# Kernel tuning notes

Hardware: AMD Instinct MI355X
Metric: run time of the kernel (lower is better)

## Reference

```python
import jax, jax.numpy as jnp
import numpy as np

N_HEADS = 16


def setup_inputs() -> dict:
    key = jax.random.key(0)
    k1, k2, k3 = jax.random.split(key, 3)
    B, S, D = 2, 2048, 1024
    x = jax.random.normal(k1, (B, S, D), dtype=jnp.float32)
    w_qkv = jax.random.normal(k2, (D, 3 * D), dtype=jnp.float32) * 0.02
    b_qkv = jnp.zeros((3 * D,), dtype=jnp.float32)
    w_proj = jax.random.normal(k3, (D, D), dtype=jnp.float32) * 0.02
    b_proj = jnp.zeros((D,), dtype=jnp.float32)
    return {"x": x, "w_qkv": w_qkv, "b_qkv": b_qkv, "w_proj": w_proj, "b_proj": b_proj}


def reference(x, w_qkv, b_qkv, w_proj, b_proj):
    # Faithful to CausalAttention.flash_atttention: the blockwise online-softmax
    # loop computes exactly softmax(Q K^T / sqrt(hd) + causal_mask) V (no dropout).
    B, S, D = x.shape
    H = N_HEADS
    hd = D // H
    scale = 1.0 / jnp.sqrt(jnp.asarray(hd, dtype=x.dtype))

    qkv = x @ w_qkv + b_qkv                       # [B, S, 3D]
    q, k, v = jnp.split(qkv, 3, axis=-1)
    q = q.reshape(B, S, H, hd).transpose(0, 2, 1, 3)  # [B, H, S, hd]
    k = k.reshape(B, S, H, hd).transpose(0, 2, 1, 3)
    v = v.reshape(B, S, H, hd).transpose(0, 2, 1, 3)

    scores = jnp.einsum('bhqd,bhkd->bhqk', q, k) * scale  # [B, H, S, S]
    causal = jnp.tril(jnp.ones((S, S), dtype=bool))
    scores = jnp.where(causal, scores, -jnp.inf)
    attn = jax.nn.softmax(scores, axis=-1)
    out = jnp.einsum('bhqk,bhkd->bhqd', attn, v)  # [B, H, S, hd]
    out = out.transpose(0, 2, 1, 3).reshape(B, S, D)
    return out @ w_proj + b_proj
```

## Files before the change

### kernel.cpp

```cpp
#include <hip/hip_runtime.h>
#include <hip/hip_bf16.h>

typedef unsigned short u16;
typedef __attribute__((ext_vector_type(8))) short short8;
typedef __attribute__((ext_vector_type(4))) float floatx4;
typedef __attribute__((ext_vector_type(16))) float floatx16;

__device__ __forceinline__ u16 f2bf(float f) {
  union { float f; unsigned u; } v; v.f = f;
  unsigned r = v.u + 0x7fffu + ((v.u >> 16) & 1u);
  return (u16)(r >> 16);
}

__device__ __forceinline__ floatx4 mfma16(short8 a, short8 b, floatx4 c) {
  return __builtin_amdgcn_mfma_f32_16x16x32_bf16(a, b, c, 0, 0, 0);
}
__device__ __forceinline__ floatx16 mfma32(short8 a, short8 b, floatx16 c) {
  return __builtin_amdgcn_mfma_f32_32x32x16_bf16(a, b, c, 0, 0, 0);
}

#define AS1 __attribute__((address_space(1)))
#define AS3 __attribute__((address_space(3)))
__device__ __forceinline__ void gload_lds16(const u16* g, u16* l) {
  __builtin_amdgcn_global_load_lds((const AS1 void*)g, (AS3 void*)l, 16, 0, 0);
}

__device__ __forceinline__ unsigned pack2(float a, float b) {
  union { __hip_bfloat162 h; unsigned u; } x;
  x.h = __hip_bfloat162(__float2bfloat16(a), __float2bfloat16(b));
  return x.u;
}

__device__ __forceinline__ float fexp2(float x) {
#if __has_builtin(__builtin_amdgcn_exp2f)
  return __builtin_amdgcn_exp2f(x);
#else
  return exp2f(x);
#endif
}

#define WAIT_VM(N) asm volatile("s_waitcnt vmcnt(" #N ")" ::: "memory")
#define BARRIER()                      \
  do {                                 \
    __builtin_amdgcn_s_barrier();      \
    asm volatile("" ::: "memory");     \
  } while (0)

#define QSCALE 0.18033688f

__global__ void __launch_bounds__(256) f32_to_bf16_vec(
    const float* __restrict__ in, u16* __restrict__ out) {
  const int i = blockIdx.x * 256 + threadIdx.x;
  const float4* p = (const float4*)in + (size_t)i * 2;
  float4 a = p[0], b = p[1];
  short8 o;
  o[0] = (short)f2bf(a.x); o[1] = (short)f2bf(a.y);
  o[2] = (short)f2bf(a.z); o[3] = (short)f2bf(a.w);
  o[4] = (short)f2bf(b.x); o[5] = (short)f2bf(b.y);
  o[6] = (short)f2bf(b.z); o[7] = (short)f2bf(b.w);
  *(short8*)(out + (size_t)i * 8) = o;
}

__global__ void __launch_bounds__(256) transpose_f32_to_bf16(
    const float* __restrict__ in, u16* __restrict__ out, int R, int C) {
  __shared__ float tile[64][65];
  const int c0 = blockIdx.x * 64, r0 = blockIdx.y * 64;
  const int t = threadIdx.x;
  const int rr = t >> 2, cc = (t & 3) * 16;
  const float* src = in + (size_t)(r0 + rr) * C + (c0 + cc);
  float4 v0 = *(const float4*)(src);
  float4 v1 = *(const float4*)(src + 4);
  float4 v2 = *(const float4*)(src + 8);
  float4 v3 = *(const float4*)(src + 12);
  tile[rr][cc + 0] = v0.x;  tile[rr][cc + 1] = v0.y;
  tile[rr][cc + 2] = v0.z;  tile[rr][cc + 3] = v0.w;
  tile[rr][cc + 4] = v1.x;  tile[rr][cc + 5] = v1.y;
  tile[rr][cc + 6] = v1.z;  tile[rr][cc + 7] = v1.w;
  tile[rr][cc + 8] = v2.x;  tile[rr][cc + 9] = v2.y;
  tile[rr][cc + 10] = v2.z; tile[rr][cc + 11] = v2.w;
  tile[rr][cc + 12] = v3.x; tile[rr][cc + 13] = v3.y;
  tile[rr][cc + 14] = v3.z; tile[rr][cc + 15] = v3.w;
  __syncthreads();
  short8 w0, w1;
#pragma unroll
  for (int i = 0; i < 8; ++i) {
    w0[i] = (short)f2bf(tile[cc + i][rr]);
    w1[i] = (short)f2bf(tile[cc + 8 + i][rr]);
  }
  u16* dst = out + (size_t)(c0 + rr) * R + (r0 + cc);
  *(short8*)dst = w0;
  *(short8*)(dst + 8) = w1;
}

__global__ void __launch_bounds__(256) gemm_qkv(
    const u16* __restrict__ A, const u16* __restrict__ Bt,
    const float* __restrict__ bias, u16* __restrict__ O0,
    u16* __restrict__ O1, u16* __restrict__ O2, int N, int K) {
  __shared__ u16 As[2][4096];
  __shared__ u16 Bs[2][4096];
  const int t = threadIdx.x, w = t >> 6, l = t & 63;
  const int lo = l & 15, g = l >> 4;
  const int wr = w >> 1, wc = w & 1;
  const int m0 = blockIdx.y * 128, n0 = blockIdx.x * 128;
  const int srow = l >> 2;
  const int schunk = (l & 3) ^ ((l >> 4) & 3);
  const u16* ApS = A + (size_t)(m0 + w * 32 + srow) * K + schunk * 8;
  const u16* BpS = Bt + (size_t)(n0 + w * 32 + srow) * K + schunk * 8;

  floatx4 acc[4][4] = {};
  const int NT = K >> 5;

#define STAGE_G(buf, kt_)                                                    \
  do {                                                                       \
    const size_t k0_ = (size_t)(kt_) * 32;                                   \
    _Pragma("unroll") for (int i = 0; i < 2; ++i)                            \
        gload_lds16(ApS + (size_t)i * 16 * K + k0_,                          \
                    &As[buf][(w * 2 + i) * 512]);                            \
    _Pragma("unroll") for (int i = 0; i < 2; ++i)                            \
        gload_lds16(BpS + (size_t)i * 16 * K + k0_,                          \
                    &Bs[buf][(w * 2 + i) * 512]);                            \
  } while (0)

#define COMPUTE_G(cur)                                                       \
  do {                                                                       \
    short8 af[4], bff[4];                                                    \
    _Pragma("unroll") for (int m = 0; m < 4; ++m) {                          \
      const int row = wr * 64 + m * 16 + lo;                                 \
      const int sl = g ^ ((lo >> 2) & 3);                                    \
      af[m] = *(const short8*)(&As[cur][row * 32 + sl * 8]);                 \
    }                                                                        \
    _Pragma("unroll") for (int n = 0; n < 4; ++n) {                          \
      const int row = wc * 64 + n * 16 + lo;                                 \
      const int sl = g ^ ((lo >> 2) & 3);                                    \
      bff[n] = *(const short8*)(&Bs[cur][row * 32 + sl * 8]);                \
    }                                                                        \
    __builtin_amdgcn_s_setprio(1);                                           \
    _Pragma("unroll") for (int m = 0; m < 4; ++m)                            \
        _Pragma("unroll") for (int n = 0; n < 4; ++n) acc[m][n] =            \
            mfma16(af[m], bff[n], acc[m][n]);                                \
    __builtin_amdgcn_s_setprio(0);                                           \
  } while (0)

  STAGE_G(0, 0);
  int cur = 0;
  for (int kt = 0; kt < NT - 1; ++kt) {
    STAGE_G(cur ^ 1, kt + 1);
    WAIT_VM(4);
    BARRIER();
    COMPUTE_G(cur);
    BARRIER();
    cur ^= 1;
  }
  WAIT_VM(0);
  BARRIER();
  COMPUTE_G(cur);
#undef STAGE_G
#undef COMPUTE_G

#pragma unroll
  for (int m = 0; m < 4; ++m) {
    const int row_base = m0 + wr * 64 + m * 16 + g * 4;
#pragma unroll
    for (int n = 0; n < 4; ++n) {
      const int col = n0 + wc * 64 + n * 16 + lo;
      const float bv = bias[col];
#pragma unroll
      for (int j = 0; j < 4; ++j) {
        const int r = row_base + j;
        const float v = acc[m][n][j] + bv;
        const int b = r >> 11, s = r & 2047;
        int c = col;
        if (c < 1024) {
          const int hh = c >> 6, d = c & 63;
          O0[(((size_t)(b * 16 + hh)) * 2048 + s) * 64 + d] = f2bf(v * QSCALE);
        } else if (c < 2048) {
          c -= 1024;
          const int hh = c >> 6, d = c & 63;
          O1[(((size_t)(b * 16 + hh)) * 2048 + s) * 64 + d] = f2bf(v);
        } else {
          c -= 2048;
          const int hh = c >> 6, d = c & 63;
          O2[(((size_t)(b * 16 + hh)) * 64 + d) * 2048 + s] = f2bf(v);
        }
      }
    }
  }
}

__global__ void __launch_bounds__(256, 2) gemm_proj(
    const u16* __restrict__ A, const u16* __restrict__ Bt,
    const float* __restrict__ bias, float* __restrict__ Of, int N, int K) {
  __shared__ u16 As[2][8192];
  __shared__ u16 Bs[2][8192];
  const int t = threadIdx.x, w = t >> 6, l = t & 63;
  const int lo = l & 15, g = l >> 4;
  const int wr = w >> 1, wc = w & 1;
  const int m0 = blockIdx.y * 128, n0 = blockIdx.x * 128;
  const int srow = l >> 3;
  const int schunk = (l & 7) ^ srow;
  const u16* ApS = A + (size_t)(m0 + w * 32 + srow) * K + schunk * 8;
  const u16* BpS = Bt + (size_t)(n0 + w * 32 + srow) * K + schunk * 8;

  floatx4 acc[4][4] = {};
  const int NT = K >> 6;

#define STAGE_P(buf, kt_)                                                    \
  do {                                                                       \
    const size_t k0_ = (size_t)(kt_) * 64;                                   \
    _Pragma("unroll") for (int i = 0; i < 4; ++i)                            \
        gload_lds16(ApS + (size_t)i * 8 * K + k0_,                           \
                    &As[buf][(w * 4 + i) * 512]);                            \
    _Pragma("unroll") for (int i = 0; i < 4; ++i)                            \
        gload_lds16(BpS + (size_t)i * 8 * K + k0_,                           \
                    &Bs[buf][(w * 4 + i) * 512]);                            \
  } while (0)

#define COMPUTE_P(cur)                                                       \
  do {                                                                       \
    short8 af[2][4], bff[2][4];                                              \
    _Pragma("unroll") for (int kk = 0; kk < 2; ++kk)                         \
        _Pragma("unroll") for (int m = 0; m < 4; ++m) {                      \
      const int row = wr * 64 + m * 16 + lo;                                 \
      const int sl = (kk * 4 + g) ^ (row & 7);                               \
      af[kk][m] = *(const short8*)(&As[cur][row * 64 + sl * 8]);             \
    }                                                                        \
    _Pragma("unroll") for (int kk = 0; kk < 2; ++kk)                         \
        _Pragma("unroll") for (int n = 0; n < 4; ++n) {                      \
      const int row = wc * 64 + n * 16 + lo;                                 \
      const int sl = (kk * 4 + g) ^ (row & 7);                               \
      bff[kk][n] = *(const short8*)(&Bs[cur][row * 64 + sl * 8]);            \
    }                                                                        \
    __builtin_amdgcn_s_setprio(1);                                           \
    _Pragma("unroll") for (int kk = 0; kk < 2; ++kk)                         \
        _Pragma("unroll") for (int m = 0; m < 4; ++m)                        \
            _Pragma("unroll") for (int n = 0; n < 4; ++n) acc[m][n] =        \
                mfma16(af[kk][m], bff[kk][n], acc[m][n]);                    \
    __builtin_amdgcn_s_setprio(0);                                           \
  } while (0)

  STAGE_P(0, 0);
  int cur = 0;
  for (int kt = 0; kt < NT - 1; ++kt) {
    STAGE_P(cur ^ 1, kt + 1);
    WAIT_VM(8);
    BARRIER();
    COMPUTE_P(cur);
    BARRIER();
    cur ^= 1;
  }
  WAIT_VM(0);
  BARRIER();
  COMPUTE_P(cur);
#undef STAGE_P
#undef COMPUTE_P

#pragma unroll
  for (int m = 0; m < 4; ++m) {
    const int row_base = m0 + wr * 64 + m * 16 + g * 4;
#pragma unroll
    for (int n = 0; n < 4; ++n) {
      const int col = n0 + wc * 64 + n * 16 + lo;
      const float bv = bias[col];
#pragma unroll
      for (int j = 0; j < 4; ++j) {
        const int r = row_base + j;
        __builtin_nontemporal_store(acc[m][n][j] + bv,
                                    &Of[(size_t)r * N + col]);
      }
    }
  }
}

__global__ void __launch_bounds__(256, 2) attn_kernel(
    const u16* __restrict__ Q, const u16* __restrict__ K,
    const u16* __restrict__ Vt, u16* __restrict__ O) {
  const int S = 2048;
  __shared__ u16 smem[2][16384];
  const int t = threadIdx.x, w = t >> 6, l = t & 63;
  const int lo = l & 31, h = l >> 5;
  const int wg = blockIdx.x;
  const int j = wg >> 1, p = wg & 1;
  const int bh = j >> 3;
  const int r = j & 7;
  const int qb = p ? (15 - r) : r;
  const int q0w = qb * 128 + w * 32;
  const int qabs = q0w + lo;
  const u16* Qb = Q + (size_t)bh * S * 64;
  const u16* Kb = K + (size_t)bh * S * 64;
  const u16* Vb = Vt + (size_t)bh * 64 * S;

  short8 qf[4];
#pragma unroll
  for (int ks = 0; ks < 4; ++ks)
    qf[ks] = *(const short8*)(Qb + (size_t)(q0w + lo) * 64 + ks * 16 + h * 8);

  floatx16 o0 = {}, o1 = {};
  float ll = 0.f;

  auto STAGE = [&](int buf, int tile) {
    const int kv0 = tile * 128;
#pragma unroll
    for (int i = 0; i < 4; ++i) {
      const int idx = i * 256 + t;
      const int rw = idx >> 3;
      const int cg = (idx & 7) ^ (rw & 7);
      gload_lds16(Kb + (size_t)(kv0 + rw) * 64 + cg * 8,
                  &smem[buf][(i * 256 + w * 64) * 8]);
    }
#pragma unroll
    for (int i = 0; i < 4; ++i) {
      const int idx = i * 256 + t;
      const int rw = idx >> 4;
      const int cg = (idx & 15) ^ (rw & 15);
      gload_lds16(Vb + (size_t)rw * S + kv0 + cg * 8,
                  &smem[buf][8192 + (i * 256 + w * 64) * 8]);
    }
  };

  auto COMPUTE = [&](int cur, int kv0) {
    floatx16 st[4] = {};
    __builtin_amdgcn_s_setprio(1);
#pragma unroll
    for (int ks = 0; ks < 4; ++ks)
#pragma unroll
      for (int nt = 0; nt < 4; ++nt) {
        const int row = nt * 32 + lo;
        short8 kf = *(const short8*)(
            &smem[cur][row * 64 + (((ks * 2 + h) ^ (row & 7)) * 8)]);
        st[nt] = mfma32(kf, qf[ks], st[nt]);
      }
    __builtin_amdgcn_s_setprio(0);
    const bool diag = (kv0 + 127 > q0w);
    float p2[4][16];
#pragma unroll
    for (int nt = 0; nt < 4; ++nt)
#pragma unroll
      for (int rr = 0; rr < 16; ++rr) {
        float v = st[nt][rr];
        if (diag) {
          const int kvr = kv0 + nt * 32 + (rr & 3) + 8 * (rr >> 2) + 4 * h;
          if (kvr > qabs) v = -1e30f;
        }
        const float e = fexp2(v);
        p2[nt][rr] = e;
        ll += e;
      }
    __builtin_amdgcn_s_setprio(1);
#pragma unroll
    for (int s = 0; s < 8; ++s) {
      const int nt = s >> 1, rb = (s & 1) * 8;
      const unsigned wA = pack2(p2[nt][rb + 0], p2[nt][rb + 1]);
      const unsigned wB = pack2(p2[nt][rb + 2], p2[nt][rb + 3]);
      const unsigned wC = pack2(p2[nt][rb + 4], p2[nt][rb + 5]);
      const unsigned wD = pack2(p2[nt][rb + 6], p2[nt][rb + 7]);
      union { unsigned u[4]; short8 s8; } bf;
#if __has_builtin(__builtin_amdgcn_permlane32_swap)
      auto r02 = __builtin_amdgcn_permlane32_swap((int)wA, (int)wC, false, false);
      auto r13 = __builtin_amdgcn_permlane32_swap((int)wB, (int)wD, false, false);
      bf.u[0] = (unsigned)r02[0];
      bf.u[1] = (unsigned)r13[0];
      bf.u[2] = (unsigned)r02[1];
      bf.u[3] = (unsigned)r13[1];
#else
      const unsigned sA = (unsigned)__shfl_xor((int)wA, 32);
      const unsigned sB = (unsigned)__shfl_xor((int)wB, 32);
      const unsigned sC = (unsigned)__shfl_xor((int)wC, 32);
      const unsigned sD = (unsigned)__shfl_xor((int)wD, 32);
      bf.u[0] = h ? sC : wA;
      bf.u[1] = h ? sD : wB;
      bf.u[2] = h ? wC : sA;
      bf.u[3] = h ? wD : sB;
#endif
      {
        const int d = lo;
        short8 vf = *(const short8*)(
            &smem[cur][8192 + d * 128 + (((s * 2 + h) ^ (d & 15)) * 8)]);
        o0 = mfma32(vf, bf.s8, o0);
      }
      {
        const int d = 32 + lo;
        short8 vf = *(const short8*)(
            &smem[cur][8192 + d * 128 + (((s * 2 + h) ^ (d & 15)) * 8)]);
        o1 = mfma32(vf, bf.s8, o1);
      }
    }
    __builtin_amdgcn_s_setprio(0);
  };

  const int T = qb + 1;
  STAGE(0, 0);
  int cur = 0;
  for (int tt = 0; tt < T - 1; ++tt) {
    STAGE(cur ^ 1, tt + 1);
    WAIT_VM(8);
    BARRIER();
    COMPUTE(cur, tt * 128);
    BARRIER();
    cur ^= 1;
  }
  WAIT_VM(0);
  BARRIER();
  COMPUTE(cur, (T - 1) * 128);
  __syncthreads();

  ll += __shfl_xor(ll, 32);
  const float rl = 1.0f / ll;
  u16* ep = &smem[0][w * 2048];
#pragma unroll
  for (int rr = 0; rr < 16; ++rr) {
    const int d0 = (rr & 3) + 8 * (rr >> 2) + 4 * h;
    ep[lo * 64 + (d0 ^ ((lo & 7) << 3))] = f2bf(o0[rr] * rl);
    const int d1 = d0 + 32;
    ep[lo * 64 + (d1 ^ ((lo & 7) << 3))] = f2bf(o1[rr] * rl);
  }
  __builtin_amdgcn_s_barrier();
  const int hh = bh & 15, b = bh >> 4;
  u16* Ob = O + ((size_t)(b * 2048 + q0w)) * 1024 + hh * 64;
#pragma unroll
  for (int pp = 0; pp < 4; ++pp) {
    const int idx = pp * 64 + l;
    const int row = idx >> 3, c = idx & 7;
    short8 v = *(const short8*)(&ep[row * 64 + ((c * 8) ^ ((row & 7) << 3))]);
    *(short8*)(Ob + (size_t)row * 1024 + c * 8) = v;
  }
}

extern "C" void kernel_launch(void* const* d_in, const int* in_sizes, int n_in,
                              void* d_out, int out_size, void* d_ws,
                              size_t ws_size, hipStream_t stream) {
  const float* x = (const float*)d_in[0];
  const float* w_qkv = (const float*)d_in[1];
  const float* b_qkv = (const float*)d_in[2];
  const float* w_proj = (const float*)d_in[3];
  const float* b_proj = (const float*)d_in[4];
  float* out = (float*)d_out;

  char* ws = (char*)d_ws;
  u16* Xb = (u16*)(ws);
  u16* WqkvT = (u16*)(ws + 8388608);
  u16* WprojT = (u16*)(ws + 14680064);
  u16* Qw = (u16*)(ws + 16777216);
  u16* Kw = (u16*)(ws + 25165824);
  u16* Vtw = (u16*)(ws + 33554432);
  u16* AttnO = Xb;

  f32_to_bf16_vec<<<2048, 256, 0, stream>>>(x, Xb);
  transpose_f32_to_bf16<<<dim3(48, 16), 256, 0, stream>>>(w_qkv, WqkvT, 1024,
                                                          3072);
  transpose_f32_to_bf16<<<dim3(16, 16), 256, 0, stream>>>(w_proj, WprojT, 1024,
                                                          1024);
  gemm_qkv<<<dim3(24, 32), 256, 0, stream>>>(Xb, WqkvT, b_qkv, Qw, Kw, Vtw,
                                             3072, 1024);
  attn_kernel<<<512, 256, 0, stream>>>(Qw, Kw, Vtw, AttnO);
  gemm_proj<<<dim3(8, 32), 256, 0, stream>>>(AttnO, WprojT, b_proj, out, 1024,
                                             1024);
}
```

Measured before the change: 134.5 us.

## Merge weight transposes, remap attention block order, split softmax sum chains

Merges the two weight-transpose launches into a single kernel that picks its matrix from the block index, removing one kernel launch. It also changes the attention grid mapping so consecutive blocks cover different batch-heads and pair light and heavy causal query blocks in a new order, which may change load balance and L2 locality. The row-sum accumulation is split into several independent partial sums to shorten the dependent add chain. Summing in a different order can change rounding slightly.

```diff
diff --git a/kernel.cpp b/kernel.cpp
--- a/kernel.cpp
+++ b/kernel.cpp
@@ -61,10 +61,22 @@
   *(short8*)(out + (size_t)i * 8) = o;
 }
 
-__global__ void __launch_bounds__(256) transpose_f32_to_bf16(
-    const float* __restrict__ in, u16* __restrict__ out, int R, int C) {
+__global__ void __launch_bounds__(256) transpose_both(
+    const float* __restrict__ wqkv, u16* __restrict__ oqkv,
+    const float* __restrict__ wproj, u16* __restrict__ oproj) {
+  const int id = blockIdx.x;
+  const float* in;
+  u16* out;
+  int R, C, bx, by;
+  if (id < 768) {
+    in = wqkv; out = oqkv; R = 1024; C = 3072;
+    bx = id % 48; by = id / 48;
+  } else {
+    in = wproj; out = oproj; R = 1024; C = 1024;
+    bx = (id - 768) % 16; by = (id - 768) / 16;
+  }
   __shared__ float tile[64][65];
-  const int c0 = blockIdx.x * 64, r0 = blockIdx.y * 64;
+  const int c0 = bx * 64, r0 = by * 64;
   const int t = threadIdx.x;
   const int rr = t >> 2, cc = (t & 3) * 16;
   const float* src = in + (size_t)(r0 + rr) * C + (c0 + cc);
@@ -279,10 +291,9 @@
   const int t = threadIdx.x, w = t >> 6, l = t & 63;
   const int lo = l & 31, h = l >> 5;
   const int wg = blockIdx.x;
-  const int j = wg >> 1, p = wg & 1;
-  const int bh = j >> 3;
-  const int r = j & 7;
-  const int qb = p ? (15 - r) : r;
+  const int bh = (wg & 7) * 4 + ((wg >> 3) & 3);
+  const int qidx = wg >> 5;
+  const int qb = (qidx < 8) ? qidx : 23 - qidx;
   const int q0w = qb * 128 + w * 32;
   const int qabs = q0w + lo;
   const u16* Qb = Q + (size_t)bh * S * 64;
@@ -295,7 +306,7 @@
     qf[ks] = *(const short8*)(Qb + (size_t)(q0w + lo) * 64 + ks * 16 + h * 8);
 
   floatx16 o0 = {}, o1 = {};
-  float ll = 0.f;
+  float lacc[4] = {0.f, 0.f, 0.f, 0.f};
 
   auto STAGE = [&](int buf, int tile) {
     const int kv0 = tile * 128;
@@ -333,7 +344,8 @@
     const bool diag = (kv0 + 127 > q0w);
     float p2[4][16];
 #pragma unroll
-    for (int nt = 0; nt < 4; ++nt)
+    for (int nt = 0; nt < 4; ++nt) {
+      float s0 = 0.f, s1 = 0.f;
 #pragma unroll
       for (int rr = 0; rr < 16; ++rr) {
         float v = st[nt][rr];
@@ -343,8 +355,10 @@
         }
         const float e = fexp2(v);
         p2[nt][rr] = e;
-        ll += e;
-      }
+        if (rr & 1) s1 += e; else s0 += e;
+      }
+      lacc[nt] += s0 + s1;
+    }
     __builtin_amdgcn_s_setprio(1);
 #pragma unroll
     for (int s = 0; s < 8; ++s) {
@@ -403,6 +417,7 @@
   COMPUTE(cur, (T - 1) * 128);
   __syncthreads();
 
+  float ll = (lacc[0] + lacc[1]) + (lacc[2] + lacc[3]);
   ll += __shfl_xor(ll, 32);
   const float rl = 1.0f / ll;
   u16* ep = &smem[0][w * 2048];
@@ -445,10 +460,7 @@
   u16* AttnO = Xb;
 
   f32_to_bf16_vec<<<2048, 256, 0, stream>>>(x, Xb);
-  transpose_f32_to_bf16<<<dim3(48, 16), 256, 0, stream>>>(w_qkv, WqkvT, 1024,
-                                                          3072);
-  transpose_f32_to_bf16<<<dim3(16, 16), 256, 0, stream>>>(w_proj, WprojT, 1024,
-                                                          1024);
+  transpose_both<<<1024, 256, 0, stream>>>(w_qkv, WqkvT, w_proj, WprojT);
   gemm_qkv<<<dim3(24, 32), 256, 0, stream>>>(Xb, WqkvT, b_qkv, Qw, Kw, Vtw,
                                              3072, 1024);
   attn_kernel<<<512, 256, 0, stream>>>(Qw, Kw, Vtw, AttnO);
```

Measured after the change: 127.1 us. 1.06x faster.
